# Kernel tuning notes

Hardware: AMD Instinct MI355X
Metric: run time of the kernel (lower is better)

Reference implementation:

```python
import jax, jax.numpy as jnp
import numpy as np

N_HEADS = 16
EPS = 1e-12  # torch F.normalize eps


def setup_inputs() -> dict:
    key = jax.random.key(0)
    ks = jax.random.split(key, 10)
    bs, qlen, dim = 2, 2048, 1024
    s = 1.0 / np.sqrt(dim)
    inp = {
        "x": jax.random.normal(ks[0], (bs, qlen, dim), dtype=jnp.float32),
        "mask": jnp.ones((bs, qlen), dtype=jnp.int32),
        "Wq": jax.random.normal(ks[1], (dim, dim), dtype=jnp.float32) * s,
        "bq": jnp.zeros((dim,), dtype=jnp.float32),
        "Wk": jax.random.normal(ks[2], (dim, dim), dtype=jnp.float32) * s,
        "bk": jnp.zeros((dim,), dtype=jnp.float32),
        "Wv": jax.random.normal(ks[3], (dim, dim), dtype=jnp.float32) * s,
        "bv": jnp.zeros((dim,), dtype=jnp.float32),
        "Wo": jax.random.normal(ks[4], (dim, dim), dtype=jnp.float32) * s,
        "bo": jnp.zeros((dim,), dtype=jnp.float32),
        "scale": jnp.asarray(1.0 / np.sqrt(dim // N_HEADS), dtype=jnp.float32),
    }
    return inp


def reference(x, mask, Wq, bq, Wk, bk, Wv, bv, Wo, bo, scale):
    bs, qlen, dim = x.shape
    dph = dim // N_HEADS

    def shape_heads(t):  # [b, s, dim] -> [b, h, s, dph]
        return t.reshape(bs, -1, N_HEADS, dph).transpose(0, 2, 1, 3)

    q = shape_heads(x @ Wq + bq)
    k = shape_heads(x @ Wk + bk)
    v = shape_heads(x @ Wv + bv)

    # cosine attention: L2-normalize q, k; learned scalar scale
    q = q / jnp.maximum(jnp.linalg.norm(q, axis=-1, keepdims=True), EPS)
    k = k / jnp.maximum(jnp.linalg.norm(k, axis=-1, keepdims=True), EPS)
    q = q * scale

    scores = jnp.einsum("bhqd,bhkd->bhqk", q, k)  # [b,h,q,k]
    pad = (mask == 0)[:, None, None, :]  # [b,1,1,k]
    scores = jnp.where(pad, -jnp.inf, scores)
    weights = jax.nn.softmax(scores.astype(jnp.float32), axis=-1).astype(scores.dtype)
    ctx = jnp.einsum("bhqk,bhkd->bhqd", weights, v)
    ctx = ctx.transpose(0, 2, 1, 3).reshape(bs, qlen, dim)
    return ctx @ Wo + bo
```

## Files before the change

### kernel.cpp

```cpp
#include <hip/hip_runtime.h>
#include <math.h>

#define SEQ 2048
#define DIM 1024
#define NH 16
#define DPH 64
#define MTOT 4096

typedef __attribute__((ext_vector_type(8))) short bf16x8;
typedef __attribute__((ext_vector_type(4))) float f32x4;
typedef __attribute__((ext_vector_type(16))) float f32x16;
typedef __attribute__((ext_vector_type(4))) unsigned int u32x4;

__device__ __forceinline__ unsigned short f2bf(float f) {
    unsigned int u = __float_as_uint(f);
    return (unsigned short)((u + 0x7FFFu + ((u >> 16) & 1u)) >> 16);
}
__device__ __forceinline__ float bf2f(unsigned short h) {
    return __uint_as_float(((unsigned int)h) << 16);
}

__device__ __forceinline__ void stage16(const void* g, void* lds) {
    __builtin_amdgcn_global_load_lds((const __attribute__((address_space(1))) void*)g,
                                     (__attribute__((address_space(3))) void*)lds,
                                     16, 0, 0);
}

__device__ __forceinline__ unsigned cvtpk(float lo, float hi) {
    unsigned w;
    asm("v_cvt_pk_bf16_f32 %0, %1, %2" : "=v"(w) : "v"(lo), "v"(hi));
    return w;
}
__device__ __forceinline__ void plswap(unsigned &a, unsigned &b) {
    asm("v_permlane32_swap_b32 %0, %1" : "+v"(a), "+v"(b));
}

__device__ __forceinline__ void xcd_remap(int gx, int gy, int gz,
                                          int &x, int &y, int &z)
{
    const int h = (blockIdx.z * gy + blockIdx.y) * gx + blockIdx.x;
    const int nb = gx * gy * gz;
    const int chunk = nb >> 3;
    const int l = (h & 7) * chunk + (h >> 3);
    const int P = gx * gz;
    y = l / P;
    const int r = l - y * P;
    z = r / gx;
    x = r - z * gx;
}

__global__ __launch_bounds__(256) void cast_x(const float* __restrict__ X,
                                              unsigned short* __restrict__ Xb)
{
    size_t i = (size_t)blockIdx.x * 256 + threadIdx.x;
    float4 v = *(const float4*)&X[i * 4];
    ushort4 o;
    o.x = f2bf(v.x); o.y = f2bf(v.y); o.z = f2bf(v.z); o.w = f2bf(v.w);
    *(ushort4*)&Xb[i * 4] = o;
}

__global__ __launch_bounds__(256) void prep_w(
    const float* __restrict__ Wq, const float* __restrict__ Wk,
    const float* __restrict__ Wv, const float* __restrict__ Wo,
    unsigned short* __restrict__ Wqt, unsigned short* __restrict__ Wkt,
    unsigned short* __restrict__ Wvt, unsigned short* __restrict__ Wot)
{
    const float* W; unsigned short* Wt;
    switch (blockIdx.z) {
        case 0: W = Wq; Wt = Wqt; break;
        case 1: W = Wk; Wt = Wkt; break;
        case 2: W = Wv; Wt = Wvt; break;
        default: W = Wo; Wt = Wot; break;
    }
    __shared__ float T[32][33];
    const int t = threadIdx.x;
    const int kt0 = blockIdx.y * 32;
    const int nt0 = blockIdx.x * 32;
    const int r = t >> 3, c4 = (t & 7) * 4;
    float4 v = *(const float4*)&W[(size_t)(kt0 + r) * DIM + nt0 + c4];
    T[r][c4 + 0] = v.x; T[r][c4 + 1] = v.y; T[r][c4 + 2] = v.z; T[r][c4 + 3] = v.w;
    __syncthreads();
    ushort4 o;
    o.x = f2bf(T[c4 + 0][r]);
    o.y = f2bf(T[c4 + 1][r]);
    o.z = f2bf(T[c4 + 2][r]);
    o.w = f2bf(T[c4 + 3][r]);
    *(ushort4*)&Wt[(size_t)(nt0 + r) * DIM + kt0 + c4] = o;
}

__global__ __launch_bounds__(256) void pack_mask(const int* __restrict__ mask,
                                                 unsigned long long* __restrict__ MB)
{
    const int w = blockIdx.x * 4 + (threadIdx.x >> 6);
    const int lane = threadIdx.x & 63;
    const int b = w >> 5, kt = w & 31;
    int m = mask[b * SEQ + kt * 64 + lane];
    unsigned long long bits = __ballot(m != 0);
    if (lane == 0) MB[w] = bits;
}

__device__ __forceinline__ void gemm_core(
    const unsigned short* __restrict__ Ab, const unsigned short* __restrict__ Bt,
    const float* __restrict__ bias, unsigned short* __restrict__ Cb,
    float* __restrict__ Cf, int mode, int bx, int by, float qs)
{
    __shared__ __align__(16) unsigned short As[2][4096];
    __shared__ __align__(16) unsigned short Bs[2][4096];

    const int tid = threadIdx.x;
    const int l = tid & 63;
    const int w = tid >> 6;
    const int wm = w >> 1, wn = w & 1;
    const int lr = l & 15, lg = l >> 4;
    const int bm = by * 128;
    const int bn = bx * 128;

    const unsigned short* a_src0 = Ab + (size_t)(bm + (2 * w) * 16 + lr) * DIM + lg * 8;
    const unsigned short* a_src1 = Ab + (size_t)(bm + (2 * w + 1) * 16 + lr) * DIM + lg * 8;
    const unsigned short* b_src0 = Bt + (size_t)(bn + (2 * w) * 16 + lr) * DIM + lg * 8;
    const unsigned short* b_src1 = Bt + (size_t)(bn + (2 * w + 1) * 16 + lr) * DIM + lg * 8;

    f32x4 acc[4][4];
#pragma unroll
    for (int i = 0; i < 4; ++i)
#pragma unroll
        for (int j = 0; j < 4; ++j) acc[i][j] = (f32x4){0.f, 0.f, 0.f, 0.f};

    stage16(a_src0, &As[0][(2 * w) * 512]);
    stage16(a_src1, &As[0][(2 * w + 1) * 512]);
    stage16(b_src0, &Bs[0][(2 * w) * 512]);
    stage16(b_src1, &Bs[0][(2 * w + 1) * 512]);

    int t = 0;
    for (int kk = 0; kk < DIM; kk += 32) {
        __syncthreads();
        if (kk + 32 < DIM) {
            const int nxt = t ^ 1;
            stage16(a_src0 + kk + 32, &As[nxt][(2 * w) * 512]);
            stage16(a_src1 + kk + 32, &As[nxt][(2 * w + 1) * 512]);
            stage16(b_src0 + kk + 32, &Bs[nxt][(2 * w) * 512]);
            stage16(b_src1 + kk + 32, &Bs[nxt][(2 * w + 1) * 512]);
        }
        bf16x8 aF[4], bF[4];
#pragma unroll
        for (int i = 0; i < 4; ++i) {
            aF[i] = *(const bf16x8*)&As[t][(wm * 4 + i) * 512 + l * 8];
            bF[i] = *(const bf16x8*)&Bs[t][(wn * 4 + i) * 512 + l * 8];
        }
#pragma unroll
        for (int i = 0; i < 4; ++i)
#pragma unroll
            for (int j = 0; j < 4; ++j)
                acc[i][j] = __builtin_amdgcn_mfma_f32_16x16x32_bf16(aF[i], bF[j], acc[i][j], 0, 0, 0);
        t ^= 1;
    }

    float bvj[4];
#pragma unroll
    for (int j = 0; j < 4; ++j) bvj[j] = bias[bn + wn * 64 + j * 16 + lr];
#pragma unroll
    for (int i = 0; i < 4; ++i)
#pragma unroll
        for (int j = 0; j < 4; ++j)
#pragma unroll
            for (int p = 0; p < 4; ++p) acc[i][j][p] += bvj[j];

    if (mode == 0) {
#pragma unroll
        for (int i = 0; i < 4; ++i) {
            float scl[4];
#pragma unroll
            for (int p = 0; p < 4; ++p) {
                float s = 0.f;
#pragma unroll
                for (int j = 0; j < 4; ++j) s = fmaf(acc[i][j][p], acc[i][j][p], s);
                s += __shfl_xor(s, 1);
                s += __shfl_xor(s, 2);
                s += __shfl_xor(s, 4);
                s += __shfl_xor(s, 8);
                scl[p] = qs / fmaxf(sqrtf(s), 1e-12f);
            }
            const int m0 = bm + wm * 64 + i * 16 + lg * 4;
#pragma unroll
            for (int j = 0; j < 4; ++j) {
                const int n = bn + wn * 64 + j * 16 + lr;
#pragma unroll
                for (int p = 0; p < 4; ++p)
                    Cb[(size_t)(m0 + p) * DIM + n] = f2bf(acc[i][j][p] * scl[p]);
            }
        }
    } else if (mode == 1) {
#pragma unroll
        for (int i = 0; i < 4; ++i) {
            const int m0 = bm + wm * 64 + i * 16 + lg * 4;
            const int b = m0 >> 11, s = m0 & 2047;
#pragma unroll
            for (int j = 0; j < 4; ++j) {
                const int n = bn + wn * 64 + j * 16 + lr;
                const int h = n >> 6, d = n & 63;
                ushort4 o;
                o.x = f2bf(acc[i][j][0]);
                o.y = f2bf(acc[i][j][1]);
                o.z = f2bf(acc[i][j][2]);
                o.w = f2bf(acc[i][j][3]);
                *(ushort4*)&Cb[((size_t)((b * NH + h) * DPH + d)) * SEQ + s] = o;
            }
        }
    } else {
#pragma unroll
        for (int i = 0; i < 4; ++i) {
            const int m0 = bm + wm * 64 + i * 16 + lg * 4;
#pragma unroll
            for (int j = 0; j < 4; ++j) {
                const int n = bn + wn * 64 + j * 16 + lr;
#pragma unroll
                for (int p = 0; p < 4; ++p)
                    Cf[(size_t)(m0 + p) * DIM + n] = acc[i][j][p];
            }
        }
    }
}

__global__ __launch_bounds__(256) void qkv_gemm(
    const unsigned short* __restrict__ Xb,
    const unsigned short* __restrict__ Wqt, const unsigned short* __restrict__ Wkt,
    const unsigned short* __restrict__ Wvt,
    const float* __restrict__ bq, const float* __restrict__ bk, const float* __restrict__ bv,
    const float* __restrict__ scale_p,
    unsigned short* __restrict__ Qb, unsigned short* __restrict__ Kb,
    unsigned short* __restrict__ Vtb)
{
    int x, y, z;
    xcd_remap(8, 32, 3, x, y, z);
    if (z == 0)
        gemm_core(Xb, Wqt, bq, Qb, nullptr, 0, x, y, scale_p[0] * 1.44269504088896340736f);
    else if (z == 1)
        gemm_core(Xb, Wkt, bk, Kb, nullptr, 0, x, y, 1.0f);
    else
        gemm_core(Xb, Wvt, bv, Vtb, nullptr, 1, x, y, 1.0f);
}

__global__ __launch_bounds__(256) void o_gemm(
    const unsigned short* __restrict__ Ab, const unsigned short* __restrict__ Wot,
    const float* __restrict__ bo, float* __restrict__ Out)
{
    int x, y, z;
    xcd_remap(8, 32, 1, x, y, z);
    gemm_core(Ab, Wot, bo, nullptr, Out, 2, x, y, 1.0f);
}

__global__ __launch_bounds__(256) void attn(
    const unsigned short* __restrict__ Qb, const unsigned short* __restrict__ Kb,
    const unsigned short* __restrict__ Vtb, const unsigned long long* __restrict__ MB,
    unsigned short* __restrict__ CTXb)
{
    __shared__ __align__(16) unsigned short Ks[2][4096];
    __shared__ __align__(16) unsigned short Vts[2][4096];

    const int tid = threadIdx.x;
    const int l = tid & 63;
    const int w = tid >> 6;
    const int l31 = l & 31;
    const int hi = l >> 5;

    int qt, h, b;
    {
        const int hh = (blockIdx.z * 16 + blockIdx.y) * 16 + blockIdx.x;
        const int ll = (hh & 7) * 64 + (hh >> 3);
        qt = ll & 15;
        const int g = ll >> 4;
        h = g & 15;
        b = g >> 4;
    }

    const size_t qrow = (size_t)(b * SEQ + qt * 128 + w * 32 + l31);
    bf16x8 qf[4];
#pragma unroll
    for (int df = 0; df < 4; ++df)
        qf[df] = *(const bf16x8*)&Qb[qrow * DIM + h * DPH + df * 16 + hi * 8];

    const int sub = l >> 3, ss = (l & 7) ^ sub;
    const unsigned short* Kptr  = Kb  + (size_t)(b * SEQ) * DIM + h * DPH;
    const unsigned short* Vtptr = Vtb + ((size_t)(b * NH + h) * DPH) * SEQ;
    const unsigned long long* mbp = MB + b * 32;

    f32x16 ctx0 = {}, ctx1 = {};
    float lsum = 0.f;

    {
        const int r0 = w * 16, r1 = w * 16 + 8;
        stage16(Kptr + (size_t)(r0 + sub) * DIM + ss * 8, &Ks[0][r0 * 64]);
        stage16(Kptr + (size_t)(r1 + sub) * DIM + ss * 8, &Ks[0][r1 * 64]);
        stage16(Vtptr + (size_t)(r0 + sub) * SEQ + ss * 8, &Vts[0][r0 * 64]);
        stage16(Vtptr + (size_t)(r1 + sub) * SEQ + ss * 8, &Vts[0][r1 * 64]);
    }

    for (int kt = 0; kt < SEQ / 64; ++kt) {
        __syncthreads();
        const int cur = kt & 1;
        if (kt + 1 < SEQ / 64) {
            const int nxt = cur ^ 1;
            const int r0 = w * 16, r1 = w * 16 + 8;
            const size_t ko = (size_t)((kt + 1) * 64);
            stage16(Kptr + (ko + r0 + sub) * DIM + ss * 8, &Ks[nxt][r0 * 64]);
            stage16(Kptr + (ko + r1 + sub) * DIM + ss * 8, &Ks[nxt][r1 * 64]);
            stage16(Vtptr + (size_t)(r0 + sub) * SEQ + ko + ss * 8, &Vts[nxt][r0 * 64]);
            stage16(Vtptr + (size_t)(r1 + sub) * SEQ + ko + ss * 8, &Vts[nxt][r1 * 64]);
        }

        const char* kbase = (const char*)Ks[cur];
        f32x16 S0 = {}, S1 = {};
#pragma unroll
        for (int df = 0; df < 4; ++df) {
            const int so = ((df * 2 + hi) ^ (l31 & 7)) << 4;
            bf16x8 k0 = *(const bf16x8*)(kbase + l31 * 128 + so);
            bf16x8 k1 = *(const bf16x8*)(kbase + (32 + l31) * 128 + so);
            S0 = __builtin_amdgcn_mfma_f32_32x32x16_bf16(k0, qf[df], S0, 0, 0, 0);
            S1 = __builtin_amdgcn_mfma_f32_32x32x16_bf16(k1, qf[df], S1, 0, 0, 0);
        }

        float p[32];
#pragma unroll
        for (int r = 0; r < 16; ++r) {
            p[r]      = __builtin_amdgcn_exp2f(S0[r]);
            p[16 + r] = __builtin_amdgcn_exp2f(S1[r]);
        }

        const unsigned long long bits = mbp[kt];
        if (bits != ~0ull) {
#pragma unroll
            for (int r = 0; r < 16; ++r) {
                const int key0 = (r & 3) + 8 * (r >> 2) + 4 * hi;
                p[r]      *= (float)((bits >> key0) & 1);
                p[16 + r] *= (float)((bits >> (32 + key0)) & 1);
            }
        }

#pragma unroll
        for (int r = 0; r < 32; ++r) lsum += p[r];

        bf16x8 pa[4];
#pragma unroll
        for (int krow = 0; krow < 2; ++krow) {
            const float* pp = &p[krow * 16];
            unsigned w01[4], w23[4];
#pragma unroll
            for (int a = 0; a < 4; ++a) {
                w01[a] = cvtpk(pp[4 * a + 0], pp[4 * a + 1]);
                w23[a] = cvtpk(pp[4 * a + 2], pp[4 * a + 3]);
            }
#pragma unroll
            for (int fh = 0; fh < 2; ++fh) {
                unsigned A0 = w01[2 * fh], B0 = w01[2 * fh + 1];
                unsigned A1 = w23[2 * fh], B1 = w23[2 * fh + 1];
                plswap(A0, B0);
                plswap(A1, B1);
                u32x4 tt = {A0, A1, B0, B1};
                union { u32x4 u; bf16x8 v; } cvt;
                cvt.u = tt;
                pa[krow * 2 + fh] = cvt.v;
            }
        }

        const char* vbase = (const char*)Vts[cur];
#pragma unroll
        for (int kf2 = 0; kf2 < 4; ++kf2) {
            const int so = ((kf2 * 2 + hi) ^ (l31 & 7)) << 4;
            bf16x8 v0 = *(const bf16x8*)(vbase + l31 * 128 + so);
            bf16x8 v1 = *(const bf16x8*)(vbase + (32 + l31) * 128 + so);
            ctx0 = __builtin_amdgcn_mfma_f32_32x32x16_bf16(pa[kf2], v0, ctx0, 0, 0, 0);
            ctx1 = __builtin_amdgcn_mfma_f32_32x32x16_bf16(pa[kf2], v1, ctx1, 0, 0, 0);
        }
    }

    lsum += __shfl_xor(lsum, 32);
    const float inv = 1.0f / lsum;

    const size_t orow0 = (size_t)(b * SEQ + qt * 128 + w * 32);
#pragma unroll
    for (int r = 0; r < 16; ++r) {
        const int q = (r & 3) + 8 * (r >> 2) + 4 * hi;
        const float invr = __shfl(inv, q);
        const size_t ro = (orow0 + q) * DIM + h * DPH;
        CTXb[ro + l31]      = f2bf(ctx0[r] * invr);
        CTXb[ro + 32 + l31] = f2bf(ctx1[r] * invr);
    }
}

extern "C" void kernel_launch(void* const* d_in, const int* in_sizes, int n_in,
                              void* d_out, int out_size, void* d_ws, size_t ws_size,
                              hipStream_t stream)
{
    const float* x    = (const float*)d_in[0];
    const int*   mask = (const int*)d_in[1];
    const float* Wq   = (const float*)d_in[2];
    const float* bq   = (const float*)d_in[3];
    const float* Wk   = (const float*)d_in[4];
    const float* bk   = (const float*)d_in[5];
    const float* Wv   = (const float*)d_in[6];
    const float* bv   = (const float*)d_in[7];
    const float* Wo   = (const float*)d_in[8];
    const float* bo   = (const float*)d_in[9];
    const float* scale = (const float*)d_in[10];
    float* out = (float*)d_out;

    char* p = (char*)d_ws;
    unsigned short* Xb  = (unsigned short*)p; p += (size_t)MTOT * DIM * 2;
    unsigned short* Wqt = (unsigned short*)p; p += (size_t)DIM * DIM * 2;
    unsigned short* Wkt = (unsigned short*)p; p += (size_t)DIM * DIM * 2;
    unsigned short* Wvt = (unsigned short*)p; p += (size_t)DIM * DIM * 2;
    unsigned short* Wot = (unsigned short*)p; p += (size_t)DIM * DIM * 2;
    unsigned short* Qb  = (unsigned short*)p; p += (size_t)MTOT * DIM * 2;
    unsigned short* Kb  = (unsigned short*)p; p += (size_t)MTOT * DIM * 2;
    unsigned short* Vtb = (unsigned short*)p; p += (size_t)MTOT * DIM * 2;
    unsigned short* CTXb = (unsigned short*)p; p += (size_t)MTOT * DIM * 2;
    unsigned long long* MBits = (unsigned long long*)p;

    cast_x<<<dim3(MTOT * DIM / 4 / 256), 256, 0, stream>>>(x, Xb);
    prep_w<<<dim3(32, 32, 4), 256, 0, stream>>>(Wq, Wk, Wv, Wo, Wqt, Wkt, Wvt, Wot);
    pack_mask<<<dim3(16), 256, 0, stream>>>(mask, MBits);
    qkv_gemm<<<dim3(8, 32, 3), 256, 0, stream>>>(
        Xb, Wqt, Wkt, Wvt, bq, bk, bv, scale, Qb, Kb, Vtb);
    attn<<<dim3(16, 16, 2), 256, 0, stream>>>(Qb, Kb, Vtb, MBits, CTXb);
    o_gemm<<<dim3(8, 32, 1), 256, 0, stream>>>(CTXb, Wot, bo, out);
}
```

Before: 239.6 us.

## Fuse prep kernels, retile QKV block-to-XCD mapping, raise priority around attention MFMAs

Merges the X cast, weight transpose-cast and mask packing into a single launch, removing two kernel launches and their gaps. The QKV GEMM block-to-XCD mapping changes so each XCD handles a group of row tiles across several N tiles, aiming for better L2 reuse of X and W. The attention kernel raises wave priority with s_setprio around the MFMA loops so matrix work is issued ahead of other waves. The combined prep kernel does 16 floats per thread for the cast, which could change memory access efficiency.

```diff
diff --git a/kernel.cpp b/kernel.cpp
--- a/kernel.cpp
+++ b/kernel.cpp
@@ -49,54 +49,54 @@
     x = r - z * gx;
 }
 
-__global__ __launch_bounds__(256) void cast_x(const float* __restrict__ X,
-                                              unsigned short* __restrict__ Xb)
-{
-    size_t i = (size_t)blockIdx.x * 256 + threadIdx.x;
-    float4 v = *(const float4*)&X[i * 4];
-    ushort4 o;
-    o.x = f2bf(v.x); o.y = f2bf(v.y); o.z = f2bf(v.z); o.w = f2bf(v.w);
-    *(ushort4*)&Xb[i * 4] = o;
-}
-
-__global__ __launch_bounds__(256) void prep_w(
+__global__ __launch_bounds__(256) void prep_all(
+    const float* __restrict__ X, unsigned short* __restrict__ Xb,
     const float* __restrict__ Wq, const float* __restrict__ Wk,
     const float* __restrict__ Wv, const float* __restrict__ Wo,
     unsigned short* __restrict__ Wqt, unsigned short* __restrict__ Wkt,
-    unsigned short* __restrict__ Wvt, unsigned short* __restrict__ Wot)
-{
-    const float* W; unsigned short* Wt;
-    switch (blockIdx.z) {
-        case 0: W = Wq; Wt = Wqt; break;
-        case 1: W = Wk; Wt = Wkt; break;
-        case 2: W = Wv; Wt = Wvt; break;
-        default: W = Wo; Wt = Wot; break;
-    }
-    __shared__ float T[32][33];
-    const int t = threadIdx.x;
-    const int kt0 = blockIdx.y * 32;
-    const int nt0 = blockIdx.x * 32;
-    const int r = t >> 3, c4 = (t & 7) * 4;
-    float4 v = *(const float4*)&W[(size_t)(kt0 + r) * DIM + nt0 + c4];
-    T[r][c4 + 0] = v.x; T[r][c4 + 1] = v.y; T[r][c4 + 2] = v.z; T[r][c4 + 3] = v.w;
-    __syncthreads();
-    ushort4 o;
-    o.x = f2bf(T[c4 + 0][r]);
-    o.y = f2bf(T[c4 + 1][r]);
-    o.z = f2bf(T[c4 + 2][r]);
-    o.w = f2bf(T[c4 + 3][r]);
-    *(ushort4*)&Wt[(size_t)(nt0 + r) * DIM + kt0 + c4] = o;
-}
-
-__global__ __launch_bounds__(256) void pack_mask(const int* __restrict__ mask,
-                                                 unsigned long long* __restrict__ MB)
-{
-    const int w = blockIdx.x * 4 + (threadIdx.x >> 6);
-    const int lane = threadIdx.x & 63;
-    const int b = w >> 5, kt = w & 31;
-    int m = mask[b * SEQ + kt * 64 + lane];
-    unsigned long long bits = __ballot(m != 0);
-    if (lane == 0) MB[w] = bits;
+    unsigned short* __restrict__ Wvt, unsigned short* __restrict__ Wot,
+    const int* __restrict__ mask, unsigned long long* __restrict__ MB)
+{
+    const int z = blockIdx.z;
+    if (z < 4) {
+        const float* W; unsigned short* Wt;
+        switch (z) {
+            case 0: W = Wq; Wt = Wqt; break;
+            case 1: W = Wk; Wt = Wkt; break;
+            case 2: W = Wv; Wt = Wvt; break;
+            default: W = Wo; Wt = Wot; break;
+        }
+        __shared__ float T[32][33];
+        const int t = threadIdx.x;
+        const int bx = blockIdx.x & 31, by = blockIdx.x >> 5;
+        const int kt0 = by * 32, nt0 = bx * 32;
+        const int r = t >> 3, c4 = (t & 7) * 4;
+        float4 v = *(const float4*)&W[(size_t)(kt0 + r) * DIM + nt0 + c4];
+        T[r][c4 + 0] = v.x; T[r][c4 + 1] = v.y; T[r][c4 + 2] = v.z; T[r][c4 + 3] = v.w;
+        __syncthreads();
+        ushort4 o;
+        o.x = f2bf(T[c4 + 0][r]);
+        o.y = f2bf(T[c4 + 1][r]);
+        o.z = f2bf(T[c4 + 2][r]);
+        o.w = f2bf(T[c4 + 3][r]);
+        *(ushort4*)&Wt[(size_t)(nt0 + r) * DIM + kt0 + c4] = o;
+    } else {
+        const size_t base = ((size_t)blockIdx.x * 256 + threadIdx.x) * 16;
+#pragma unroll
+        for (int q = 0; q < 4; ++q) {
+            float4 v = *(const float4*)&X[base + q * 4];
+            ushort4 o;
+            o.x = f2bf(v.x); o.y = f2bf(v.y); o.z = f2bf(v.z); o.w = f2bf(v.w);
+            *(ushort4*)&Xb[base + q * 4] = o;
+        }
+        if (blockIdx.x < 16) {
+            const int w = blockIdx.x * 4 + (threadIdx.x >> 6);
+            const int lane = threadIdx.x & 63;
+            const int b = w >> 5, kt = w & 31;
+            unsigned long long bits = __ballot(mask[b * SEQ + kt * 64 + lane] != 0);
+            if (lane == 0) MB[w] = bits;
+        }
+    }
 }
 
 __device__ __forceinline__ void gemm_core(
@@ -231,7 +231,17 @@
     unsigned short* __restrict__ Vtb)
 {
     int x, y, z;
-    xcd_remap(8, 32, 3, x, y, z);
+    {
+        const int h = (blockIdx.z * 32 + blockIdx.y) * 8 + blockIdx.x;
+        const int xcd = h & 7;
+        const int idx = h >> 3;
+        const int xzg = xcd & 1, yg = xcd >> 1;
+        const int lxz = idx % 12, ly = idx / 12;
+        const int xz = xzg * 12 + lxz;
+        x = xz & 7;
+        z = xz >> 3;
+        y = yg * 8 + ly;
+    }
     if (z == 0)
         gemm_core(Xb, Wqt, bq, Qb, nullptr, 0, x, y, scale_p[0] * 1.44269504088896340736f);
     else if (z == 1)
@@ -310,6 +320,7 @@
 
         const char* kbase = (const char*)Ks[cur];
         f32x16 S0 = {}, S1 = {};
+        __builtin_amdgcn_s_setprio(1);
 #pragma unroll
         for (int df = 0; df < 4; ++df) {
             const int so = ((df * 2 + hi) ^ (l31 & 7)) << 4;
@@ -318,6 +329,7 @@
             S0 = __builtin_amdgcn_mfma_f32_32x32x16_bf16(k0, qf[df], S0, 0, 0, 0);
             S1 = __builtin_amdgcn_mfma_f32_32x32x16_bf16(k1, qf[df], S1, 0, 0, 0);
         }
+        __builtin_amdgcn_s_setprio(0);
 
         float p[32];
 #pragma unroll
@@ -363,6 +375,7 @@
         }
 
         const char* vbase = (const char*)Vts[cur];
+        __builtin_amdgcn_s_setprio(1);
 #pragma unroll
         for (int kf2 = 0; kf2 < 4; ++kf2) {
             const int so = ((kf2 * 2 + hi) ^ (l31 & 7)) << 4;
@@ -371,6 +384,7 @@
             ctx0 = __builtin_amdgcn_mfma_f32_32x32x16_bf16(pa[kf2], v0, ctx0, 0, 0, 0);
             ctx1 = __builtin_amdgcn_mfma_f32_32x32x16_bf16(pa[kf2], v1, ctx1, 0, 0, 0);
         }
+        __builtin_amdgcn_s_setprio(0);
     }
 
     lsum += __shfl_xor(lsum, 32);
@@ -416,9 +430,8 @@
     unsigned short* CTXb = (unsigned short*)p; p += (size_t)MTOT * DIM * 2;
     unsigned long long* MBits = (unsigned long long*)p;
 
-    cast_x<<<dim3(MTOT * DIM / 4 / 256), 256, 0, stream>>>(x, Xb);
-    prep_w<<<dim3(32, 32, 4), 256, 0, stream>>>(Wq, Wk, Wv, Wo, Wqt, Wkt, Wvt, Wot);
-    pack_mask<<<dim3(16), 256, 0, stream>>>(mask, MBits);
+    prep_all<<<dim3(1024, 1, 5), 256, 0, stream>>>(
+        x, Xb, Wq, Wk, Wv, Wo, Wqt, Wkt, Wvt, Wot, mask, MBits);
     qkv_gemm<<<dim3(8, 32, 3), 256, 0, stream>>>(
         Xb, Wqt, Wkt, Wvt, bq, bk, bv, scale, Qb, Kb, Vtb);
     attn<<<dim3(16, 16, 2), 256, 0, stream>>>(Qb, Kb, Vtb, MBits, CTXb);
```

Measured after the change: 237.0 us. No clear change (-1.1%).
